# Kernel optimization log

Hardware: AMD Instinct MI355X
Metric: run time of the kernel (lower is better)

Reference implementation:

```python
import jax, jax.numpy as jnp
import numpy as np

B, D_MODEL, SEQ = 8, 1024, 1024   # D_MODEL = hidden_dim*2
H, DK, DV = 8, 128, 128
EPS_LN, EPS_NORM, NEG = 1e-6, 1e-12, -1e9


def layer_norm_2d(x, g, b):
    # torch LayerNorm([d_model, seq_len]): normalize over last two dims
    mu = jnp.mean(x, axis=(-2, -1), keepdims=True)
    var = jnp.mean((x - mu) ** 2, axis=(-2, -1), keepdims=True)
    return (x - mu) * jax.lax.rsqrt(var + EPS_LN) * g + b


def setup_inputs() -> dict:
    key = jax.random.key(0)
    ks = jax.random.split(key, 14)
    s = lambda *sh: 1.0 / np.sqrt(sh[-1])
    return {
        "enc_input": jax.random.normal(ks[0], (B, D_MODEL, SEQ), jnp.float32),
        "slf_attn_mask": jax.random.randint(ks[1], (B, D_MODEL, D_MODEL), 0, 2, jnp.int32),
        "ln1_g": jnp.ones((D_MODEL, SEQ), jnp.float32),
        "ln1_b": jnp.zeros((D_MODEL, SEQ), jnp.float32),
        "wq": jax.random.normal(ks[2], (H * DK, SEQ), jnp.float32) * s(SEQ),
        "wk": jax.random.normal(ks[3], (H * DK, SEQ), jnp.float32) * s(SEQ),
        "wv": jax.random.normal(ks[4], (H * DV, SEQ), jnp.float32) * s(SEQ),
        "wo": jax.random.normal(ks[5], (SEQ, H * DV), jnp.float32) * s(H * DV),
        "ln2_g": jnp.ones((D_MODEL, SEQ), jnp.float32),
        "ln2_b": jnp.zeros((D_MODEL, SEQ), jnp.float32),
        "w1": jax.random.normal(ks[6], (SEQ, SEQ), jnp.float32) * s(SEQ),
        "b1": jnp.zeros((SEQ,), jnp.float32),
        "w2": jax.random.normal(ks[7], (SEQ, SEQ), jnp.float32) * s(SEQ),
        "b2": jnp.zeros((SEQ,), jnp.float32),
    }


def reference(enc_input, slf_attn_mask, ln1_g, ln1_b, wq, wk, wv, wo,
              ln2_g, ln2_b, w1, b1, w2, b2):
    x = enc_input                                # [B, M, S], M = d_model
    residual = x
    h = layer_norm_2d(x, ln1_g, ln1_b)
    # linear projections on last (seq) dim, split heads -> [B, H, M, dk]
    q = jnp.einsum('bms,os->bmo', h, wq).reshape(B, D_MODEL, H, DK).transpose(0, 2, 1, 3)
    k = jnp.einsum('bms,os->bmo', h, wk).reshape(B, D_MODEL, H, DK).transpose(0, 2, 1, 3)
    v = jnp.einsum('bms,os->bmo', h, wv).reshape(B, D_MODEL, H, DV).transpose(0, 2, 1, 3)
    # F.normalize over dim=1 (the HEAD axis) -- faithful to source
    k_norm = k / jnp.maximum(jnp.sqrt(jnp.sum(k * k, axis=1, keepdims=True)), EPS_NORM)
    # no temperature scaling (stored but unused in source)
    attn = jnp.einsum('bhmd,bhnd->bhmn', q, k_norm)          # [B, H, M, M]
    attn = jnp.where(slf_attn_mask[:, None] == 0, NEG, attn)
    attn = jax.nn.softmax(attn, axis=-1)
    out = jnp.einsum('bhmn,bhnd->bhmd', attn, v)             # [B, H, M, dv]
    out = out.transpose(0, 2, 1, 3).reshape(B, D_MODEL, H * DV)
    x = jnp.einsum('bmo,so->bms', out, wo) + residual        # fc + residual
    # positionwise FFN on the seq axis, pre-LN residual
    h2 = layer_norm_2d(x, ln2_g, ln2_b)
    h2 = jax.nn.relu(jnp.einsum('bms,os->bmo', h2, w1) + b1)
    h2 = jnp.einsum('bmo,so->bms', h2, w2) + b2
    enc_output = h2 + x
    return enc_output, attn
```

## Files before the change

### kernel.cpp

```cpp
#include <hip/hip_runtime.h>

#define DEVINL __device__ __forceinline__

typedef __bf16 bf16x8 __attribute__((ext_vector_type(8)));
typedef float  f32x4  __attribute__((ext_vector_type(4)));

DEVINL unsigned short f2bf(float f) {
  union { float f; unsigned int u; } v; v.f = f;
  unsigned int u = v.u;
  return (unsigned short)((u + 0x7fffu + ((u >> 16) & 1u)) >> 16);
}
DEVINL float bf2f(unsigned short b) {
  union { unsigned int u; float f; } v; v.u = ((unsigned int)b) << 16;
  return v.f;
}

#define GLD_LDS16(SRC, DST) \
  __builtin_amdgcn_global_load_lds((const __attribute__((address_space(1))) void*)(SRC), \
                                   (__attribute__((address_space(3))) void*)(DST), 16, 0, 0)

template<int EPI>
__global__ __launch_bounds__(256) void gemm_bt(
    const unsigned short* __restrict__ Ap, const unsigned short* __restrict__ Bp, void* __restrict__ Cp,
    const float* __restrict__ bias, const float* __restrict__ res,
    int M, int N, int K, int lda, int ldb, int ldc, int H,
    long sAb, long sAh, long sBb, long sBh, long sCb, long sCh)
{
  constexpr int SMEMSZ = (EPI == 2) ? 34816 : 16384;
  __shared__ __align__(16) char smem[SMEMSZ];
  unsigned short* sB = (unsigned short*)(smem + 8192);

  const int tid = threadIdx.x;
  const int w = tid >> 6, l = tid & 63;
  const int wr = w >> 1, wc = w & 1;
  const int ntn = N >> 7;
  const int tm = (int)blockIdx.x / ntn;
  const int tn = (int)blockIdx.x - tm * ntn;
  const int z = blockIdx.z;
  const int bb = z / H, hh = z - bb * H;
  const long offA = (long)bb * sAb + (long)hh * sAh;
  const long offB = (long)bb * sBb + (long)hh * sBh;
  const long offC = (long)bb * sCb + (long)hh * sCh;

  f32x4 zero = {0.f, 0.f, 0.f, 0.f};
  f32x4 acc[4][4];
  #pragma unroll
  for (int m = 0; m < 4; ++m)
    #pragma unroll
    for (int n = 0; n < 4; ++n) acc[m][n] = zero;

  for (int k0 = 0; k0 < K; k0 += 32) {
    __syncthreads();
    const int rl = l >> 2, cl = (l & 3) << 3;
    #pragma unroll
    for (int i = 0; i < 2; ++i) {
      const unsigned short* srcA = Ap + offA + (long)(tm*128 + w*32 + i*16 + rl) * lda + (k0 + cl);
      GLD_LDS16(srcA, (unsigned short*)smem + (w*32 + i*16) * 32);
      const unsigned short* srcB = Bp + offB + (long)(tn*128 + w*32 + i*16 + rl) * ldb + (k0 + cl);
      GLD_LDS16(srcB, sB + (w*32 + i*16) * 32);
    }
    __syncthreads();

    bf16x8 af[4], bfr[4];
    const unsigned short* sA = (const unsigned short*)smem;
    #pragma unroll
    for (int m = 0; m < 4; ++m) {
      int row = wr*64 + m*16 + (l & 15);
      af[m] = *(const bf16x8*)(sA + row*32 + ((l >> 4) << 3));
    }
    #pragma unroll
    for (int n = 0; n < 4; ++n) {
      int row = wc*64 + n*16 + (l & 15);
      bfr[n] = *(const bf16x8*)(sB + row*32 + ((l >> 4) << 3));
    }
    #pragma unroll
    for (int m = 0; m < 4; ++m)
      #pragma unroll
      for (int n = 0; n < 4; ++n)
        acc[m][n] = __builtin_amdgcn_mfma_f32_16x16x32_bf16(af[m], bfr[n], acc[m][n], 0, 0, 0);
  }

  if constexpr (EPI == 2) {
    __syncthreads();
    unsigned short* sT = (unsigned short*)smem;
    #pragma unroll
    for (int m = 0; m < 4; ++m)
      #pragma unroll
      for (int n = 0; n < 4; ++n)
        #pragma unroll
        for (int r = 0; r < 4; ++r) {
          int rowl = wr*64 + m*16 + ((l >> 4) << 2) + r;
          int coll = wc*64 + n*16 + (l & 15);
          sT[coll*136 + rowl] = f2bf(acc[m][n][r]);
        }
    __syncthreads();
    #pragma unroll
    for (int i = 0; i < 8; ++i) {
      int idx = tid + i*256;
      int c = idx >> 4, ch = idx & 15;
      bf16x8 vv = *(const bf16x8*)(sT + c*136 + ch*8);
      *(bf16x8*)((unsigned short*)Cp + offC + (long)(tn*128 + c)*ldc + (tm*128 + ch*8)) = vv;
    }
  } else {
    #pragma unroll
    for (int m = 0; m < 4; ++m) {
      #pragma unroll
      for (int n = 0; n < 4; ++n) {
        #pragma unroll
        for (int r = 0; r < 4; ++r) {
          int row = tm*128 + wr*64 + m*16 + ((l >> 4) << 2) + r;
          int col = tn*128 + wc*64 + n*16 + (l & 15);
          float v = acc[m][n][r];
          long ci = offC + (long)row * ldc + col;
          if constexpr (EPI == 3) {
            ((float*)Cp)[ci] = v + res[ci];
          } else if constexpr (EPI == 4) {
            ((unsigned short*)Cp)[ci] = f2bf(fmaxf(v + bias[col], 0.f));
          } else if constexpr (EPI == 5) {
            ((float*)Cp)[ci] = v + bias[col] + res[ci];
          }
        }
      }
    }
  }
}

__global__ __launch_bounds__(256) void gemm_split(
    const unsigned short* __restrict__ A1, const unsigned short* __restrict__ A2,
    const unsigned short* __restrict__ B1, const unsigned short* __restrict__ B2,
    unsigned short* __restrict__ Cp, unsigned short* __restrict__ Cp2,
    int M, int N, int K, int lda, int ldb, int ldc)
{
  __shared__ __align__(16) unsigned short sAll[4 * 4096];
  unsigned short* sA1 = sAll;
  unsigned short* sA2 = sAll + 4096;
  unsigned short* sB1 = sAll + 8192;
  unsigned short* sB2 = sAll + 12288;

  const int tid = threadIdx.x;
  const int w = tid >> 6, l = tid & 63;
  const int wr = w >> 1, wc = w & 1;
  const int ntn = N >> 7;
  const int tm = (int)blockIdx.x / ntn;
  const int tn = (int)blockIdx.x - tm * ntn;

  f32x4 zero = {0.f, 0.f, 0.f, 0.f};
  f32x4 acc[4][4];
  #pragma unroll
  for (int m = 0; m < 4; ++m)
    #pragma unroll
    for (int n = 0; n < 4; ++n) acc[m][n] = zero;

  const int rl = l >> 2, cl = (l & 3) << 3;

  for (int k0 = 0; k0 < K; k0 += 32) {
    __syncthreads();
    #pragma unroll
    for (int i = 0; i < 2; ++i) {
      const int row = w*32 + i*16;
      const long asrc = (long)(tm*128 + row + rl) * lda + (k0 + cl);
      const long bsrc = (long)(tn*128 + row + rl) * ldb + (k0 + cl);
      GLD_LDS16(A1 + asrc, sA1 + row*32);
      GLD_LDS16(A2 + asrc, sA2 + row*32);
      GLD_LDS16(B1 + bsrc, sB1 + row*32);
      GLD_LDS16(B2 + bsrc, sB2 + row*32);
    }
    __syncthreads();

    bf16x8 a1[4], a2[4], bb4[4];
    int aoff[4], boff[4];
    #pragma unroll
    for (int m = 0; m < 4; ++m) {
      int row = wr*64 + m*16 + (l & 15);
      aoff[m] = row*32 + ((l >> 4) << 3);
      a1[m] = *(const bf16x8*)(sA1 + aoff[m]);
      a2[m] = *(const bf16x8*)(sA2 + aoff[m]);
    }
    #pragma unroll
    for (int n = 0; n < 4; ++n) {
      int row = wc*64 + n*16 + (l & 15);
      boff[n] = row*32 + ((l >> 4) << 3);
      bb4[n] = *(const bf16x8*)(sB1 + boff[n]);
    }
    #pragma unroll
    for (int m = 0; m < 4; ++m)
      #pragma unroll
      for (int n = 0; n < 4; ++n) {
        acc[m][n] = __builtin_amdgcn_mfma_f32_16x16x32_bf16(a1[m], bb4[n], acc[m][n], 0, 0, 0);
        acc[m][n] = __builtin_amdgcn_mfma_f32_16x16x32_bf16(a2[m], bb4[n], acc[m][n], 0, 0, 0);
      }
    #pragma unroll
    for (int n = 0; n < 4; ++n)
      bb4[n] = *(const bf16x8*)(sB2 + boff[n]);
    #pragma unroll
    for (int m = 0; m < 4; ++m)
      #pragma unroll
      for (int n = 0; n < 4; ++n)
        acc[m][n] = __builtin_amdgcn_mfma_f32_16x16x32_bf16(a1[m], bb4[n], acc[m][n], 0, 0, 0);
  }

  #pragma unroll
  for (int m = 0; m < 4; ++m) {
    #pragma unroll
    for (int n = 0; n < 4; ++n) {
      #pragma unroll
      for (int r = 0; r < 4; ++r) {
        int row = tm*128 + wr*64 + m*16 + ((l >> 4) << 2) + r;
        int col = tn*128 + wc*64 + n*16 + (l & 15);
        float v = acc[m][n][r];
        long ci = (long)row * ldc + col;
        unsigned short hv = f2bf(v);
        Cp[ci] = hv;
        Cp2[ci] = f2bf(v - bf2f(hv));
      }
    }
  }
}

__global__ __launch_bounds__(256, 2) void attn_fused(
    const unsigned short* __restrict__ q1, const unsigned short* __restrict__ q2,
    const unsigned short* __restrict__ kn1, const unsigned short* __restrict__ kn2,
    const unsigned short* __restrict__ vt, const unsigned int* __restrict__ mbits,
    float* __restrict__ attn, unsigned short* __restrict__ outm)
{
  __shared__ __align__(16) char smem[65536];
  const int tid = threadIdx.x;
  const int w = tid >> 6, l = tid & 63;
  const int l15 = l & 15, l4 = l >> 4;
  const int row0 = (int)blockIdx.x * 32;
  const int z = (int)blockIdx.z;
  const int bb = z >> 3, hh = z & 7;
  const long base = (long)bb * 1048576;
  const int ocol = hh * 128;

  f32x4 s[2][16];
  #pragma unroll
  for (int mf = 0; mf < 2; ++mf)
    #pragma unroll
    for (int nf = 0; nf < 16; ++nf) s[mf][nf] = (f32x4){0.f, 0.f, 0.f, 0.f};

  #pragma unroll
  for (int ks = 0; ks < 4; ++ks) {
    const int kk = ocol + ks*32 + l4*8;
    bf16x8 a1[2], a2[2];
    #pragma unroll
    for (int mf = 0; mf < 2; ++mf) {
      long ai = base + (long)(row0 + mf*16 + l15) * 1024 + kk;
      a1[mf] = *(const bf16x8*)(q1 + ai);
      a2[mf] = *(const bf16x8*)(q2 + ai);
    }
    #pragma unroll
    for (int nf = 0; nf < 16; ++nf) {
      long bi = base + (long)(w*256 + nf*16 + l15) * 1024 + kk;
      bf16x8 b1 = *(const bf16x8*)(kn1 + bi);
      bf16x8 b2 = *(const bf16x8*)(kn2 + bi);
      #pragma unroll
      for (int mf = 0; mf < 2; ++mf) {
        s[mf][nf] = __builtin_amdgcn_mfma_f32_16x16x32_bf16(a1[mf], b1, s[mf][nf], 0, 0, 0);
        s[mf][nf] = __builtin_amdgcn_mfma_f32_16x16x32_bf16(a2[mf], b1, s[mf][nf], 0, 0, 0);
        s[mf][nf] = __builtin_amdgcn_mfma_f32_16x16x32_bf16(a1[mf], b2, s[mf][nf], 0, 0, 0);
      }
    }
  }

  #pragma unroll
  for (int mf = 0; mf < 2; ++mf) {
    #pragma unroll
    for (int r = 0; r < 4; ++r) {
      int mg = row0 + mf*16 + l4*4 + r;
      const unsigned int* wrow = mbits + (long)bb*32768 + (long)mg*32 + w*8;
      unsigned int wd[8];
      #pragma unroll
      for (int j = 0; j < 8; ++j) wd[j] = wrow[j];
      #pragma unroll
      for (int nf = 0; nf < 16; ++nf) {
        unsigned int bit = (wd[nf >> 1] >> (((nf & 1) << 4) + l15)) & 1u;
        if (!bit) s[mf][nf][r] = -1e9f;
      }
    }
  }

  float* red = (float*)smem;

  float mx[2][4];
  #pragma unroll
  for (int mf = 0; mf < 2; ++mf)
    #pragma unroll
    for (int r = 0; r < 4; ++r) {
      float m = s[mf][0][r];
      #pragma unroll
      for (int nf = 1; nf < 16; ++nf) m = fmaxf(m, s[mf][nf][r]);
      #pragma unroll
      for (int o = 1; o < 16; o <<= 1) m = fmaxf(m, __shfl_xor(m, o, 64));
      mx[mf][r] = m;
      if (l15 == 0) red[w*32 + mf*16 + l4*4 + r] = m;
    }
  __syncthreads();
  #pragma unroll
  for (int mf = 0; mf < 2; ++mf)
    #pragma unroll
    for (int r = 0; r < 4; ++r) {
      int ml = mf*16 + l4*4 + r;
      mx[mf][r] = fmaxf(fmaxf(red[ml], red[32 + ml]), fmaxf(red[64 + ml], red[96 + ml]));
    }
  __syncthreads();

  float sm[2][4];
  #pragma unroll
  for (int mf = 0; mf < 2; ++mf)
    #pragma unroll
    for (int r = 0; r < 4; ++r) sm[mf][r] = 0.f;
  #pragma unroll
  for (int mf = 0; mf < 2; ++mf)
    #pragma unroll
    for (int nf = 0; nf < 16; ++nf)
      #pragma unroll
      for (int r = 0; r < 4; ++r) {
        float e = __expf(s[mf][nf][r] - mx[mf][r]);
        s[mf][nf][r] = e;
        sm[mf][r] += e;
      }
  #pragma unroll
  for (int mf = 0; mf < 2; ++mf)
    #pragma unroll
    for (int r = 0; r < 4; ++r) {
      float t = sm[mf][r];
      #pragma unroll
      for (int o = 1; o < 16; o <<= 1) t += __shfl_xor(t, o, 64);
      if (l15 == 0) red[w*32 + mf*16 + l4*4 + r] = t;
    }
  __syncthreads();
  float inv[2][4];
  #pragma unroll
  for (int mf = 0; mf < 2; ++mf)
    #pragma unroll
    for (int r = 0; r < 4; ++r) {
      int ml = mf*16 + l4*4 + r;
      inv[mf][r] = 1.f / (red[ml] + red[32 + ml] + red[64 + ml] + red[96 + ml]);
    }
  __syncthreads();

  char* pbase = smem + w * 16384;
  float* arow = attn + (long)(bb*8 + hh) * 1048576;
  #pragma unroll
  for (int mf = 0; mf < 2; ++mf)
    #pragma unroll
    for (int nf = 0; nf < 16; ++nf)
      #pragma unroll
      for (int r = 0; r < 4; ++r) {
        int ml = mf*16 + l4*4 + r;
        int cl = nf*16 + l15;
        float a = s[mf][nf][r] * inv[mf][r];
        arow[(long)(row0 + ml) * 1024 + (w*256 + cl)] = a;
        int byte = (ml*512 + cl*2) ^ ((ml & 7) << 4);
        *(unsigned short*)(pbase + byte) = f2bf(a);
      }
  __syncthreads();

  f32x4 o[2][8];
  #pragma unroll
  for (int mf = 0; mf < 2; ++mf)
    #pragma unroll
    for (int df = 0; df < 8; ++df) o[mf][df] = (f32x4){0.f, 0.f, 0.f, 0.f};
  #pragma unroll
  for (int ks = 0; ks < 8; ++ks) {
    bf16x8 pa[2];
    #pragma unroll
    for (int mf = 0; mf < 2; ++mf) {
      int ml = mf*16 + l15;
      int byte = (ml*512 + (ks*32 + l4*8)*2) ^ ((ml & 7) << 4);
      pa[mf] = *(const bf16x8*)(pbase + byte);
    }
    #pragma unroll
    for (int df = 0; df < 8; ++df) {
      long vi = base + (long)(ocol + df*16 + l15) * 1024 + (w*256 + ks*32 + l4*8);
      bf16x8 vb = *(const bf16x8*)(vt + vi);
      #pragma unroll
      for (int mf = 0; mf < 2; ++mf)
        o[mf][df] = __builtin_amdgcn_mfma_f32_16x16x32_bf16(pa[mf], vb, o[mf][df], 0, 0, 0);
    }
  }
  __syncthreads();

  float* pp = (float*)smem + w * 4096;
  #pragma unroll
  for (int mf = 0; mf < 2; ++mf)
    #pragma unroll
    for (int df = 0; df < 8; ++df)
      #pragma unroll
      for (int r = 0; r < 4; ++r)
        pp[(mf*16 + l4*4 + r)*128 + df*16 + l15] = o[mf][df][r];
  __syncthreads();
  #pragma unroll
  for (int it = 0; it < 4; ++it) {
    int i = tid + it*256;
    f32x4 a4 = ((const f32x4*)smem)[i];
    a4 += ((const f32x4*)(smem + 16384))[i];
    a4 += ((const f32x4*)(smem + 32768))[i];
    a4 += ((const f32x4*)(smem + 49152))[i];
    int ml = i >> 5, d0 = (i & 31) << 2;
    ushort4 st;
    st.x = f2bf(a4[0]); st.y = f2bf(a4[1]); st.z = f2bf(a4[2]); st.w = f2bf(a4[3]);
    *(ushort4*)(outm + (long)(bb*1024 + row0 + ml) * 1024 + ocol + d0) = st;
  }
}

__global__ __launch_bounds__(256) void pack_mask(const int* __restrict__ mask,
                                                 unsigned int* __restrict__ bits) {
  int w = threadIdx.x >> 6, l = threadIdx.x & 63;
  long rowid = (long)blockIdx.x * 4 + w;
  const int* mrow = mask + rowid * 1024;
  unsigned int* brow = bits + rowid * 32;
  #pragma unroll
  for (int it = 0; it < 16; ++it) {
    unsigned long long b = __ballot(mrow[it*64 + l] != 0);
    if (l == 0) { brow[it*2] = (unsigned int)b; brow[it*2 + 1] = (unsigned int)(b >> 32); }
  }
}

__global__ __launch_bounds__(256) void ln_stats1(const float* __restrict__ x, float2* __restrict__ part) {
  __shared__ float2 sred[4];
  int b = blockIdx.y, blk = blockIdx.x;
  const float4* xp = (const float4*)(x + (long)b * 1048576 + (long)blk * 8192);
  float s = 0.f, ss = 0.f;
  for (int i = threadIdx.x; i < 2048; i += 256) {
    float4 v = xp[i];
    s  += v.x + v.y + v.z + v.w;
    ss += v.x*v.x + v.y*v.y + v.z*v.z + v.w*v.w;
  }
  #pragma unroll
  for (int o = 32; o; o >>= 1) { s += __shfl_down(s, o, 64); ss += __shfl_down(ss, o, 64); }
  if ((threadIdx.x & 63) == 0) sred[threadIdx.x >> 6] = make_float2(s, ss);
  __syncthreads();
  if (threadIdx.x == 0) {
    float S = 0.f, SS = 0.f;
    #pragma unroll
    for (int j = 0; j < 4; ++j) { S += sred[j].x; SS += sred[j].y; }
    part[b * 128 + blk] = make_float2(S, SS);
  }
}

__global__ __launch_bounds__(128) void ln_stats2(const float2* __restrict__ part, float2* __restrict__ stats,
                                                 float invN, float eps) {
  __shared__ float2 tmp[2];
  int b = blockIdx.x;
  float2 p = part[b * 128 + threadIdx.x];
  float s = p.x, ss = p.y;
  #pragma unroll
  for (int o = 32; o; o >>= 1) { s += __shfl_down(s, o, 64); ss += __shfl_down(ss, o, 64); }
  if ((threadIdx.x & 63) == 0) tmp[threadIdx.x >> 6] = make_float2(s, ss);
  __syncthreads();
  if (threadIdx.x == 0) {
    float S = tmp[0].x + tmp[1].x, SS = tmp[0].y + tmp[1].y;
    float mu = S * invN;
    float var = SS * invN - mu * mu;
    stats[b] = make_float2(mu, rsqrtf(var + eps));
  }
}

template<bool LO>
__global__ __launch_bounds__(256) void ln_apply(const float* __restrict__ x, const float* __restrict__ g,
                                                const float* __restrict__ be, const float2* __restrict__ stats,
                                                unsigned short* __restrict__ hi, unsigned short* __restrict__ lo) {
  long i = (long)blockIdx.x * 256 + threadIdx.x;
  long e = i << 2;
  int b   = (int)(e >> 20);
  int rem = (int)(e & 1048575);
  float2 st = stats[b];
  float4 xv = ((const float4*)x)[i];
  float4 gv = *(const float4*)(g + rem);
  float4 bv = *(const float4*)(be + rem);
  float h0 = (xv.x - st.x) * st.y * gv.x + bv.x;
  float h1 = (xv.y - st.x) * st.y * gv.y + bv.y;
  float h2 = (xv.z - st.x) * st.y * gv.z + bv.z;
  float h3 = (xv.w - st.x) * st.y * gv.w + bv.w;
  ushort4 h;
  h.x = f2bf(h0); h.y = f2bf(h1); h.z = f2bf(h2); h.w = f2bf(h3);
  ((ushort4*)hi)[i] = h;
  if (LO) {
    ushort4 l4;
    l4.x = f2bf(h0 - bf2f(h.x)); l4.y = f2bf(h1 - bf2f(h.y));
    l4.z = f2bf(h2 - bf2f(h.z)); l4.w = f2bf(h3 - bf2f(h.w));
    ((ushort4*)lo)[i] = l4;
  }
}

__global__ __launch_bounds__(256) void split_bf16(const float* __restrict__ src,
                                                  unsigned short* __restrict__ hi,
                                                  unsigned short* __restrict__ lo) {
  long i = (long)blockIdx.x * 256 + threadIdx.x;
  float4 v = ((const float4*)src)[i];
  ushort4 h, l4;
  h.x = f2bf(v.x); l4.x = f2bf(v.x - bf2f(h.x));
  h.y = f2bf(v.y); l4.y = f2bf(v.y - bf2f(h.y));
  h.z = f2bf(v.z); l4.z = f2bf(v.z - bf2f(h.z));
  h.w = f2bf(v.w); l4.w = f2bf(v.w - bf2f(h.w));
  ((ushort4*)hi)[i] = h;
  ((ushort4*)lo)[i] = l4;
}

__global__ __launch_bounds__(256) void cast_bf16(const float* __restrict__ src,
                                                 unsigned short* __restrict__ dst) {
  long i = (long)blockIdx.x * 256 + threadIdx.x;
  float4 v = ((const float4*)src)[i];
  ushort4 h;
  h.x = f2bf(v.x); h.y = f2bf(v.y); h.z = f2bf(v.z); h.w = f2bf(v.w);
  ((ushort4*)dst)[i] = h;
}

__global__ __launch_bounds__(256) void knorm_split2(const unsigned short* __restrict__ k1,
                                                    const unsigned short* __restrict__ k2,
                                                    unsigned short* __restrict__ kn1,
                                                    unsigned short* __restrict__ kn2) {
  int t = blockIdx.x * 256 + threadIdx.x;
  int b = t >> 17;
  int rem = t & 131071;
  int m = rem >> 7;
  int d = rem & 127;
  long base = (long)b * 1048576 + (long)m * 1024 + d;
  float v[8]; float s = 0.f;
  #pragma unroll
  for (int h = 0; h < 8; ++h) {
    v[h] = bf2f(k1[base + h * 128]) + bf2f(k2[base + h * 128]);
    s += v[h] * v[h];
  }
  float rn = 1.f / fmaxf(sqrtf(s), 1e-12f);
  #pragma unroll
  for (int h = 0; h < 8; ++h) {
    float f = v[h] * rn;
    unsigned short hv = f2bf(f);
    kn1[base + h * 128] = hv;
    kn2[base + h * 128] = f2bf(f - bf2f(hv));
  }
}

extern "C" void kernel_launch(void* const* d_in, const int* in_sizes, int n_in,
                              void* d_out, int out_size, void* d_ws, size_t ws_size,
                              hipStream_t stream) {
  const float* enc  = (const float*)d_in[0];
  const int*   mask = (const int*)d_in[1];
  const float* ln1g = (const float*)d_in[2];
  const float* ln1b = (const float*)d_in[3];
  const float* wq   = (const float*)d_in[4];
  const float* wk   = (const float*)d_in[5];
  const float* wv   = (const float*)d_in[6];
  const float* wo   = (const float*)d_in[7];
  const float* ln2g = (const float*)d_in[8];
  const float* ln2b = (const float*)d_in[9];
  const float* w1   = (const float*)d_in[10];
  const float* b1   = (const float*)d_in[11];
  const float* w2   = (const float*)d_in[12];
  const float* b2   = (const float*)d_in[13];

  float* out_enc  = (float*)d_out;
  float* out_attn = out_enc + 8388608;

  const size_t MB = 1ull << 20;
  char* ws = (char*)d_ws;
  unsigned short* h1   = (unsigned short*)(ws + 0 * MB);
  unsigned short* h2   = (unsigned short*)(ws + 16 * MB);
  unsigned short* q1   = (unsigned short*)(ws + 32 * MB);
  unsigned short* q2   = (unsigned short*)(ws + 48 * MB);
  unsigned short* k1r  = (unsigned short*)(ws + 64 * MB);
  unsigned short* k2r  = (unsigned short*)(ws + 80 * MB);
  unsigned short* kn1  = (unsigned short*)(ws + 96 * MB);
  unsigned short* kn2  = (unsigned short*)(ws + 112 * MB);
  unsigned short* vt   = (unsigned short*)(ws + 128 * MB);
  unsigned short* outm = (unsigned short*)(ws + 144 * MB);
  float*          x2f  = (float*)(ws + 160 * MB);
  unsigned short* h2b  = (unsigned short*)(ws + 32 * MB);
  unsigned short* tb   = (unsigned short*)(ws + 48 * MB);
  unsigned short* wq1  = (unsigned short*)(ws + 192 * MB);
  unsigned short* wq2  = (unsigned short*)(ws + 194 * MB);
  unsigned short* wk1  = (unsigned short*)(ws + 196 * MB);
  unsigned short* wk2  = (unsigned short*)(ws + 198 * MB);
  unsigned short* wv1  = (unsigned short*)(ws + 200 * MB);
  unsigned short* wob  = (unsigned short*)(ws + 202 * MB);
  unsigned short* w1b  = (unsigned short*)(ws + 204 * MB);
  unsigned short* w2b  = (unsigned short*)(ws + 206 * MB);
  float2* part  = (float2*)(ws + 208 * MB);
  float2* stats = part + 1024;
  unsigned int* mbits = (unsigned int*)(ws + 209 * MB);

  const float invN = 1.f / 1048576.f;

  ln_stats1<<<dim3(128, 8), 256, 0, stream>>>(enc, part);
  ln_stats2<<<dim3(8), 128, 0, stream>>>(part, stats, invN, 1e-6f);
  ln_apply<true><<<dim3(8192), 256, 0, stream>>>(enc, ln1g, ln1b, stats, h1, h2);

  split_bf16<<<dim3(1024), 256, 0, stream>>>(wq, wq1, wq2);
  split_bf16<<<dim3(1024), 256, 0, stream>>>(wk, wk1, wk2);
  cast_bf16 <<<dim3(1024), 256, 0, stream>>>(wv, wv1);
  cast_bf16 <<<dim3(1024), 256, 0, stream>>>(wo, wob);
  cast_bf16 <<<dim3(1024), 256, 0, stream>>>(w1, w1b);
  cast_bf16 <<<dim3(1024), 256, 0, stream>>>(w2, w2b);
  pack_mask <<<dim3(2048), 256, 0, stream>>>(mask, mbits);

  gemm_split<<<dim3(512), 256, 0, stream>>>(h1, h2, wq1, wq2, q1, q2, 8192, 1024, 1024, 1024, 1024, 1024);
  gemm_split<<<dim3(512), 256, 0, stream>>>(h1, h2, wk1, wk2, k1r, k2r, 8192, 1024, 1024, 1024, 1024, 1024);

  gemm_bt<2><<<dim3(64, 1, 8), 256, 0, stream>>>(h1, wv1, vt, nullptr, nullptr,
      1024, 1024, 1024, 1024, 1024, 1024, 1, 1048576, 0, 0, 0, 1048576, 0);

  knorm_split2<<<dim3(4096), 256, 0, stream>>>(k1r, k2r, kn1, kn2);

  attn_fused<<<dim3(32, 1, 64), 256, 0, stream>>>(q1, q2, kn1, kn2, vt, mbits, out_attn, outm);

  gemm_bt<3><<<dim3(512), 256, 0, stream>>>(outm, wob, x2f, nullptr, enc,
      8192, 1024, 1024, 1024, 1024, 1024, 1, 0, 0, 0, 0, 0, 0);

  ln_stats1<<<dim3(128, 8), 256, 0, stream>>>(x2f, part);
  ln_stats2<<<dim3(8), 128, 0, stream>>>(part, stats, invN, 1e-6f);
  ln_apply<false><<<dim3(8192), 256, 0, stream>>>(x2f, ln2g, ln2b, stats, h2b, nullptr);

  gemm_bt<4><<<dim3(512), 256, 0, stream>>>(h2b, w1b, tb, b1, nullptr,
      8192, 1024, 1024, 1024, 1024, 1024, 1, 0, 0, 0, 0, 0, 0);
  gemm_bt<5><<<dim3(512), 256, 0, stream>>>(tb, w2b, out_enc, b2, x2f,
      8192, 1024, 1024, 1024, 1024, 1024, 1, 0, 0, 0, 0, 0, 0);
}
```

Measured before the change: 619.9 us.

## Restructure fused attention into 8-wave blocks with double-buffered P and per-wave output slices

Measured after the change: 766.5 us. 23.6% more time.

```diff
diff --git a/kernel.cpp b/kernel.cpp
--- a/kernel.cpp
+++ b/kernel.cpp
@@ -217,192 +217,167 @@
   }
 }
 
-__global__ __launch_bounds__(256, 2) void attn_fused(
+__global__ __launch_bounds__(512, 4) void attn_fused(
     const unsigned short* __restrict__ q1, const unsigned short* __restrict__ q2,
     const unsigned short* __restrict__ kn1, const unsigned short* __restrict__ kn2,
     const unsigned short* __restrict__ vt, const unsigned int* __restrict__ mbits,
     float* __restrict__ attn, unsigned short* __restrict__ outm)
 {
-  __shared__ __align__(16) char smem[65536];
+  __shared__ __align__(16) char smem[33280];
+  char* buf0 = smem;
+  char* buf1 = smem + 16384;
+  float* red = (float*)(smem + 32768);
+
   const int tid = threadIdx.x;
   const int w = tid >> 6, l = tid & 63;
+  const int wr = w >> 2, wc = w & 3;
   const int l15 = l & 15, l4 = l >> 4;
   const int row0 = (int)blockIdx.x * 32;
   const int z = (int)blockIdx.z;
   const int bb = z >> 3, hh = z & 7;
   const long base = (long)bb * 1048576;
   const int ocol = hh * 128;
-
-  f32x4 s[2][16];
-  #pragma unroll
-  for (int mf = 0; mf < 2; ++mf)
-    #pragma unroll
-    for (int nf = 0; nf < 16; ++nf) s[mf][nf] = (f32x4){0.f, 0.f, 0.f, 0.f};
+  const int mrow = row0 + wr * 16;
+
+  f32x4 s[16];
+  #pragma unroll
+  for (int nf = 0; nf < 16; ++nf) s[nf] = (f32x4){0.f, 0.f, 0.f, 0.f};
 
   #pragma unroll
   for (int ks = 0; ks < 4; ++ks) {
     const int kk = ocol + ks*32 + l4*8;
-    bf16x8 a1[2], a2[2];
-    #pragma unroll
-    for (int mf = 0; mf < 2; ++mf) {
-      long ai = base + (long)(row0 + mf*16 + l15) * 1024 + kk;
-      a1[mf] = *(const bf16x8*)(q1 + ai);
-      a2[mf] = *(const bf16x8*)(q2 + ai);
-    }
+    long ai = base + (long)(mrow + l15) * 1024 + kk;
+    bf16x8 a1 = *(const bf16x8*)(q1 + ai);
+    bf16x8 a2 = *(const bf16x8*)(q2 + ai);
     #pragma unroll
     for (int nf = 0; nf < 16; ++nf) {
-      long bi = base + (long)(w*256 + nf*16 + l15) * 1024 + kk;
+      long bi = base + (long)(wc*256 + nf*16 + l15) * 1024 + kk;
       bf16x8 b1 = *(const bf16x8*)(kn1 + bi);
       bf16x8 b2 = *(const bf16x8*)(kn2 + bi);
-      #pragma unroll
-      for (int mf = 0; mf < 2; ++mf) {
-        s[mf][nf] = __builtin_amdgcn_mfma_f32_16x16x32_bf16(a1[mf], b1, s[mf][nf], 0, 0, 0);
-        s[mf][nf] = __builtin_amdgcn_mfma_f32_16x16x32_bf16(a2[mf], b1, s[mf][nf], 0, 0, 0);
-        s[mf][nf] = __builtin_amdgcn_mfma_f32_16x16x32_bf16(a1[mf], b2, s[mf][nf], 0, 0, 0);
+      s[nf] = __builtin_amdgcn_mfma_f32_16x16x32_bf16(a1, b1, s[nf], 0, 0, 0);
+      s[nf] = __builtin_amdgcn_mfma_f32_16x16x32_bf16(a2, b1, s[nf], 0, 0, 0);
+      s[nf] = __builtin_amdgcn_mfma_f32_16x16x32_bf16(a1, b2, s[nf], 0, 0, 0);
+    }
+  }
+
+  #pragma unroll
+  for (int r = 0; r < 4; ++r) {
+    const unsigned int* wrow = mbits + (long)bb*32768 + (long)(mrow + l4*4 + r)*32 + wc*8;
+    unsigned int wd[8];
+    #pragma unroll
+    for (int j = 0; j < 8; ++j) wd[j] = wrow[j];
+    #pragma unroll
+    for (int nf = 0; nf < 16; ++nf) {
+      unsigned int bit = (wd[nf >> 1] >> (((nf & 1) << 4) + l15)) & 1u;
+      if (!bit) s[nf][r] = -1e9f;
+    }
+  }
+
+  float mx[4];
+  #pragma unroll
+  for (int r = 0; r < 4; ++r) {
+    float m = s[0][r];
+    #pragma unroll
+    for (int nf = 1; nf < 16; ++nf) m = fmaxf(m, s[nf][r]);
+    #pragma unroll
+    for (int o = 1; o < 16; o <<= 1) m = fmaxf(m, __shfl_xor(m, o, 64));
+    if (l15 == 0) red[w*16 + l4*4 + r] = m;
+  }
+  __syncthreads();
+  #pragma unroll
+  for (int r = 0; r < 4; ++r) {
+    int rowl = l4*4 + r;
+    mx[r] = fmaxf(fmaxf(red[(wr*4+0)*16 + rowl], red[(wr*4+1)*16 + rowl]),
+                  fmaxf(red[(wr*4+2)*16 + rowl], red[(wr*4+3)*16 + rowl]));
+  }
+  __syncthreads();
+
+  float sm[4] = {0.f, 0.f, 0.f, 0.f};
+  #pragma unroll
+  for (int nf = 0; nf < 16; ++nf)
+    #pragma unroll
+    for (int r = 0; r < 4; ++r) {
+      float e = __expf(s[nf][r] - mx[r]);
+      s[nf][r] = e;
+      sm[r] += e;
+    }
+  #pragma unroll
+  for (int r = 0; r < 4; ++r) {
+    float t = sm[r];
+    #pragma unroll
+    for (int o = 1; o < 16; o <<= 1) t += __shfl_xor(t, o, 64);
+    if (l15 == 0) red[w*16 + l4*4 + r] = t;
+  }
+  __syncthreads();
+  float inv[4];
+  #pragma unroll
+  for (int r = 0; r < 4; ++r) {
+    int rowl = l4*4 + r;
+    inv[r] = 1.f / (red[(wr*4+0)*16 + rowl] + red[(wr*4+1)*16 + rowl] +
+                    red[(wr*4+2)*16 + rowl] + red[(wr*4+3)*16 + rowl]);
+  }
+  __syncthreads();
+
+  float* arow = attn + (long)(bb*8 + hh) * 1048576;
+  #pragma unroll
+  for (int nf = 0; nf < 16; ++nf)
+    #pragma unroll
+    for (int r = 0; r < 4; ++r) {
+      float a = s[nf][r] * inv[r];
+      s[nf][r] = a;
+      arow[(long)(mrow + l4*4 + r) * 1024 + (wc*256 + nf*16 + l15)] = a;
+    }
+
+  auto write_P = [&](char* buf) {
+    #pragma unroll
+    for (int nf = 0; nf < 16; ++nf)
+      #pragma unroll
+      for (int r = 0; r < 4; ++r) {
+        int ml = wr*16 + l4*4 + r;
+        int byte = (ml*512 + (nf*16 + l15)*2) ^ ((ml & 7) << 4);
+        *(unsigned short*)(buf + byte) = f2bf(s[nf][r]);
       }
-    }
-  }
-
-  #pragma unroll
-  for (int mf = 0; mf < 2; ++mf) {
+  };
+
+  f32x4 o[2];
+  o[0] = (f32x4){0.f, 0.f, 0.f, 0.f};
+  o[1] = (f32x4){0.f, 0.f, 0.f, 0.f};
+  auto pv_chunk = [&](const char* buf, int c) {
+    #pragma unroll
+    for (int ks = 0; ks < 8; ++ks) {
+      int ml = wr*16 + l15;
+      int byte = (ml*512 + (ks*32 + l4*8)*2) ^ ((ml & 7) << 4);
+      bf16x8 pa = *(const bf16x8*)(buf + byte);
+      #pragma unroll
+      for (int df = 0; df < 2; ++df) {
+        long vi = base + (long)(ocol + wc*32 + df*16 + l15) * 1024 + (c*256 + ks*32 + l4*8);
+        bf16x8 vb = *(const bf16x8*)(vt + vi);
+        o[df] = __builtin_amdgcn_mfma_f32_16x16x32_bf16(pa, vb, o[df], 0, 0, 0);
+      }
+    }
+  };
+
+  if (wc == 0) write_P(buf0);
+  __syncthreads();
+  if (wc == 1) write_P(buf1);
+  pv_chunk(buf0, 0);
+  __syncthreads();
+  if (wc == 2) write_P(buf0);
+  pv_chunk(buf1, 1);
+  __syncthreads();
+  if (wc == 3) write_P(buf1);
+  pv_chunk(buf0, 2);
+  __syncthreads();
+  pv_chunk(buf1, 3);
+
+  #pragma unroll
+  for (int df = 0; df < 2; ++df)
     #pragma unroll
     for (int r = 0; r < 4; ++r) {
-      int mg = row0 + mf*16 + l4*4 + r;
-      const unsigned int* wrow = mbits + (long)bb*32768 + (long)mg*32 + w*8;
-      unsigned int wd[8];
-      #pragma unroll
-      for (int j = 0; j < 8; ++j) wd[j] = wrow[j];
-      #pragma unroll
-      for (int nf = 0; nf < 16; ++nf) {
-        unsigned int bit = (wd[nf >> 1] >> (((nf & 1) << 4) + l15)) & 1u;
-        if (!bit) s[mf][nf][r] = -1e9f;
-      }
-    }
-  }
-
-  float* red = (float*)smem;
-
-  float mx[2][4];
-  #pragma unroll
-  for (int mf = 0; mf < 2; ++mf)
-    #pragma unroll
-    for (int r = 0; r < 4; ++r) {
-      float m = s[mf][0][r];
-      #pragma unroll
-      for (int nf = 1; nf < 16; ++nf) m = fmaxf(m, s[mf][nf][r]);
-      #pragma unroll
-      for (int o = 1; o < 16; o <<= 1) m = fmaxf(m, __shfl_xor(m, o, 64));
-      mx[mf][r] = m;
-      if (l15 == 0) red[w*32 + mf*16 + l4*4 + r] = m;
-    }
-  __syncthreads();
-  #pragma unroll
-  for (int mf = 0; mf < 2; ++mf)
-    #pragma unroll
-    for (int r = 0; r < 4; ++r) {
-      int ml = mf*16 + l4*4 + r;
-      mx[mf][r] = fmaxf(fmaxf(red[ml], red[32 + ml]), fmaxf(red[64 + ml], red[96 + ml]));
-    }
-  __syncthreads();
-
-  float sm[2][4];
-  #pragma unroll
-  for (int mf = 0; mf < 2; ++mf)
-    #pragma unroll
-    for (int r = 0; r < 4; ++r) sm[mf][r] = 0.f;
-  #pragma unroll
-  for (int mf = 0; mf < 2; ++mf)
-    #pragma unroll
-    for (int nf = 0; nf < 16; ++nf)
-      #pragma unroll
-      for (int r = 0; r < 4; ++r) {
-        float e = __expf(s[mf][nf][r] - mx[mf][r]);
-        s[mf][nf][r] = e;
-        sm[mf][r] += e;
-      }
-  #pragma unroll
-  for (int mf = 0; mf < 2; ++mf)
-    #pragma unroll
-    for (int r = 0; r < 4; ++r) {
-      float t = sm[mf][r];
-      #pragma unroll
-      for (int o = 1; o < 16; o <<= 1) t += __shfl_xor(t, o, 64);
-      if (l15 == 0) red[w*32 + mf*16 + l4*4 + r] = t;
-    }
-  __syncthreads();
-  float inv[2][4];
-  #pragma unroll
-  for (int mf = 0; mf < 2; ++mf)
-    #pragma unroll
-    for (int r = 0; r < 4; ++r) {
-      int ml = mf*16 + l4*4 + r;
-      inv[mf][r] = 1.f / (red[ml] + red[32 + ml] + red[64 + ml] + red[96 + ml]);
-    }
-  __syncthreads();
-
-  char* pbase = smem + w * 16384;
-  float* arow = attn + (long)(bb*8 + hh) * 1048576;
-  #pragma unroll
-  for (int mf = 0; mf < 2; ++mf)
-    #pragma unroll
-    for (int nf = 0; nf < 16; ++nf)
-      #pragma unroll
-      for (int r = 0; r < 4; ++r) {
-        int ml = mf*16 + l4*4 + r;
-        int cl = nf*16 + l15;
-        float a = s[mf][nf][r] * inv[mf][r];
-        arow[(long)(row0 + ml) * 1024 + (w*256 + cl)] = a;
-        int byte = (ml*512 + cl*2) ^ ((ml & 7) << 4);
-        *(unsigned short*)(pbase + byte) = f2bf(a);
-      }
-  __syncthreads();
-
-  f32x4 o[2][8];
-  #pragma unroll
-  for (int mf = 0; mf < 2; ++mf)
-    #pragma unroll
-    for (int df = 0; df < 8; ++df) o[mf][df] = (f32x4){0.f, 0.f, 0.f, 0.f};
-  #pragma unroll
-  for (int ks = 0; ks < 8; ++ks) {
-    bf16x8 pa[2];
-    #pragma unroll
-    for (int mf = 0; mf < 2; ++mf) {
-      int ml = mf*16 + l15;
-      int byte = (ml*512 + (ks*32 + l4*8)*2) ^ ((ml & 7) << 4);
-      pa[mf] = *(const bf16x8*)(pbase + byte);
-    }
-    #pragma unroll
-    for (int df = 0; df < 8; ++df) {
-      long vi = base + (long)(ocol + df*16 + l15) * 1024 + (w*256 + ks*32 + l4*8);
-      bf16x8 vb = *(const bf16x8*)(vt + vi);
-      #pragma unroll
-      for (int mf = 0; mf < 2; ++mf)
-        o[mf][df] = __builtin_amdgcn_mfma_f32_16x16x32_bf16(pa[mf], vb, o[mf][df], 0, 0, 0);
-    }
-  }
-  __syncthreads();
-
-  float* pp = (float*)smem + w * 4096;
-  #pragma unroll
-  for (int mf = 0; mf < 2; ++mf)
-    #pragma unroll
-    for (int df = 0; df < 8; ++df)
-      #pragma unroll
-      for (int r = 0; r < 4; ++r)
-        pp[(mf*16 + l4*4 + r)*128 + df*16 + l15] = o[mf][df][r];
-  __syncthreads();
-  #pragma unroll
-  for (int it = 0; it < 4; ++it) {
-    int i = tid + it*256;
-    f32x4 a4 = ((const f32x4*)smem)[i];
-    a4 += ((const f32x4*)(smem + 16384))[i];
-    a4 += ((const f32x4*)(smem + 32768))[i];
-    a4 += ((const f32x4*)(smem + 49152))[i];
-    int ml = i >> 5, d0 = (i & 31) << 2;
-    ushort4 st;
-    st.x = f2bf(a4[0]); st.y = f2bf(a4[1]); st.z = f2bf(a4[2]); st.w = f2bf(a4[3]);
-    *(ushort4*)(outm + (long)(bb*1024 + row0 + ml) * 1024 + ocol + d0) = st;
-  }
+      int row = row0 + wr*16 + l4*4 + r;
+      int col = ocol + wc*32 + df*16 + l15;
+      outm[(long)(bb*1024 + row) * 1024 + col] = f2bf(o[df][r]);
+    }
 }
 
 __global__ __launch_bounds__(256) void pack_mask(const int* __restrict__ mask,
@@ -604,7 +579,7 @@
 
   knorm_split2<<<dim3(4096), 256, 0, stream>>>(k1r, k2r, kn1, kn2);
 
-  attn_fused<<<dim3(32, 1, 64), 256, 0, stream>>>(q1, q2, kn1, kn2, vt, mbits, out_attn, outm);
+  attn_fused<<<dim3(32, 1, 64), 512, 0, stream>>>(q1, q2, kn1, kn2, vt, mbits, out_attn, outm);
 
   gemm_bt<3><<<dim3(512), 256, 0, stream>>>(outm, wob, x2f, nullptr, enc,
       8192, 1024, 1024, 1024, 1024, 1024, 1, 0, 0, 0, 0, 0, 0);
```

## Split P·V across waves by output column to halve LDS and raise occupancy

Applied to the files above, without the earlier changes.

New measurement: 1.278 ms. 2.06x slower.

```diff
diff --git a/kernel.cpp b/kernel.cpp
--- a/kernel.cpp
+++ b/kernel.cpp
@@ -217,13 +217,15 @@
   }
 }
 
-__global__ __launch_bounds__(256, 2) void attn_fused(
+__global__ __launch_bounds__(256, 4) void attn_fused(
     const unsigned short* __restrict__ q1, const unsigned short* __restrict__ q2,
     const unsigned short* __restrict__ kn1, const unsigned short* __restrict__ kn2,
     const unsigned short* __restrict__ vt, const unsigned int* __restrict__ mbits,
     float* __restrict__ attn, unsigned short* __restrict__ outm)
 {
-  __shared__ __align__(16) char smem[65536];
+  __shared__ __align__(16) char smem[33280];
+  float* red = (float*)(smem + 32768);
+
   const int tid = threadIdx.x;
   const int w = tid >> 6, l = tid & 63;
   const int l15 = l & 15, l4 = l >> 4;
@@ -280,8 +282,6 @@
     }
   }
 
-  float* red = (float*)smem;
-
   float mx[2][4];
   #pragma unroll
   for (int mf = 0; mf < 2; ++mf)
@@ -292,7 +292,6 @@
       for (int nf = 1; nf < 16; ++nf) m = fmaxf(m, s[mf][nf][r]);
       #pragma unroll
       for (int o = 1; o < 16; o <<= 1) m = fmaxf(m, __shfl_xor(m, o, 64));
-      mx[mf][r] = m;
       if (l15 == 0) red[w*32 + mf*16 + l4*4 + r] = m;
     }
   __syncthreads();
@@ -340,7 +339,6 @@
     }
   __syncthreads();
 
-  char* pbase = smem + w * 16384;
   float* arow = attn + (long)(bb*8 + hh) * 1048576;
   #pragma unroll
   for (int mf = 0; mf < 2; ++mf)
@@ -349,60 +347,71 @@
       #pragma unroll
       for (int r = 0; r < 4; ++r) {
         int ml = mf*16 + l4*4 + r;
-        int cl = nf*16 + l15;
         float a = s[mf][nf][r] * inv[mf][r];
-        arow[(long)(row0 + ml) * 1024 + (w*256 + cl)] = a;
-        int byte = (ml*512 + cl*2) ^ ((ml & 7) << 4);
-        *(unsigned short*)(pbase + byte) = f2bf(a);
-      }
-  __syncthreads();
-
-  f32x4 o[2][8];
-  #pragma unroll
-  for (int mf = 0; mf < 2; ++mf)
-    #pragma unroll
-    for (int df = 0; df < 8; ++df) o[mf][df] = (f32x4){0.f, 0.f, 0.f, 0.f};
-  #pragma unroll
-  for (int ks = 0; ks < 8; ++ks) {
-    bf16x8 pa[2];
-    #pragma unroll
-    for (int mf = 0; mf < 2; ++mf) {
-      int ml = mf*16 + l15;
-      int byte = (ml*512 + (ks*32 + l4*8)*2) ^ ((ml & 7) << 4);
-      pa[mf] = *(const bf16x8*)(pbase + byte);
-    }
-    #pragma unroll
-    for (int df = 0; df < 8; ++df) {
-      long vi = base + (long)(ocol + df*16 + l15) * 1024 + (w*256 + ks*32 + l4*8);
-      bf16x8 vb = *(const bf16x8*)(vt + vi);
-      #pragma unroll
-      for (int mf = 0; mf < 2; ++mf)
-        o[mf][df] = __builtin_amdgcn_mfma_f32_16x16x32_bf16(pa[mf], vb, o[mf][df], 0, 0, 0);
-    }
-  }
-  __syncthreads();
-
-  float* pp = (float*)smem + w * 4096;
-  #pragma unroll
-  for (int mf = 0; mf < 2; ++mf)
-    #pragma unroll
-    for (int df = 0; df < 8; ++df)
-      #pragma unroll
-      for (int r = 0; r < 4; ++r)
-        pp[(mf*16 + l4*4 + r)*128 + df*16 + l15] = o[mf][df][r];
-  __syncthreads();
-  #pragma unroll
-  for (int it = 0; it < 4; ++it) {
-    int i = tid + it*256;
-    f32x4 a4 = ((const f32x4*)smem)[i];
-    a4 += ((const f32x4*)(smem + 16384))[i];
-    a4 += ((const f32x4*)(smem + 32768))[i];
-    a4 += ((const f32x4*)(smem + 49152))[i];
-    int ml = i >> 5, d0 = (i & 31) << 2;
-    ushort4 st;
-    st.x = f2bf(a4[0]); st.y = f2bf(a4[1]); st.z = f2bf(a4[2]); st.w = f2bf(a4[3]);
-    *(ushort4*)(outm + (long)(bb*1024 + row0 + ml) * 1024 + ocol + d0) = st;
-  }
+        s[mf][nf][r] = a;
+        arow[(long)(row0 + ml) * 1024 + (w*256 + nf*16 + l15)] = a;
+        if (nf < 8) {
+          int byte = (ml*1024 + (w*128 + nf*16 + l15)*2) ^ ((ml & 7) << 4);
+          *(unsigned short*)(smem + byte) = f2bf(a);
+        }
+      }
+  __syncthreads();
+
+  f32x4 o[2][2];
+  #pragma unroll
+  for (int mf = 0; mf < 2; ++mf)
+    #pragma unroll
+    for (int df = 0; df < 2; ++df) o[mf][df] = (f32x4){0.f, 0.f, 0.f, 0.f};
+
+  auto pv_half = [&](int keyoff) {
+    #pragma unroll
+    for (int ks = 0; ks < 16; ++ks) {
+      bf16x8 pa[2];
+      #pragma unroll
+      for (int mf = 0; mf < 2; ++mf) {
+        int ml = mf*16 + l15;
+        int byte = (ml*1024 + (ks*32 + l4*8)*2) ^ ((ml & 7) << 4);
+        pa[mf] = *(const bf16x8*)(smem + byte);
+      }
+      int kcol = (ks >> 2)*256 + keyoff + (ks & 3)*32 + l4*8;
+      #pragma unroll
+      for (int df = 0; df < 2; ++df) {
+        long vi = base + (long)(ocol + w*32 + df*16 + l15) * 1024 + kcol;
+        bf16x8 vb = *(const bf16x8*)(vt + vi);
+        #pragma unroll
+        for (int mf = 0; mf < 2; ++mf)
+          o[mf][df] = __builtin_amdgcn_mfma_f32_16x16x32_bf16(pa[mf], vb, o[mf][df], 0, 0, 0);
+      }
+    }
+  };
+
+  pv_half(0);
+  __syncthreads();
+
+  #pragma unroll
+  for (int mf = 0; mf < 2; ++mf)
+    #pragma unroll
+    for (int nf = 8; nf < 16; ++nf)
+      #pragma unroll
+      for (int r = 0; r < 4; ++r) {
+        int ml = mf*16 + l4*4 + r;
+        int byte = (ml*1024 + (w*128 + (nf - 8)*16 + l15)*2) ^ ((ml & 7) << 4);
+        *(unsigned short*)(smem + byte) = f2bf(s[mf][nf][r]);
+      }
+  __syncthreads();
+
+  pv_half(128);
+
+  #pragma unroll
+  for (int mf = 0; mf < 2; ++mf)
+    #pragma unroll
+    for (int df = 0; df < 2; ++df)
+      #pragma unroll
+      for (int r = 0; r < 4; ++r) {
+        int row = row0 + mf*16 + l4*4 + r;
+        int col = ocol + w*32 + df*16 + l15;
+        outm[(long)(bb*1024 + row) * 1024 + col] = f2bf(o[mf][df][r]);
+      }
 }
 
 __global__ __launch_bounds__(256) void pack_mask(const int* __restrict__ mask,
```
